# Kernel tuning notes

Measured on AMD Instinct MI355X. Metric: run time of the kernel, lower is better.

Reference implementation:

```python
import jax, jax.numpy as jnp
import numpy as np

B, S, L, CIN = 8, 32, 128, 1024
C1, C2 = 512, 256            # conv1_channel, conv2_channel
D1, D2 = 512, 128            # deconv1_channel, deconv2_channel
CD, SIM = 300, 128           # concept_dim, similarity_dim
L4 = L // 4


def _conv1d(x, w, b, pad):
    # x: [N, Cin, L], w: [Cout, Cin, k] (PyTorch layout)
    y = jax.lax.conv_general_dilated(x, w, (1,), [(pad, pad)],
                                     dimension_numbers=('NCH', 'OIH', 'NCH'))
    return y + b[None, :, None]


def _maxpool2(x):
    return jax.lax.reduce_window(x, -jnp.inf, jax.lax.max, (1, 1, 2), (1, 1, 2), 'VALID')


def _deconv1d(x, w, b):
    # PyTorch ConvTranspose1d(kernel=4, stride=2, padding=1); w: [Cin, Cout, k]
    w2 = jnp.flip(w, -1).transpose(1, 0, 2)  # -> OIH
    y = jax.lax.conv_general_dilated(x, w2, (1,), [(2, 2)], lhs_dilation=(2,),
                                     dimension_numbers=('NCH', 'OIH', 'NCH'))
    return y + b[None, :, None]


def setup_inputs():
    ks = jax.random.split(jax.random.key(0), 32)
    g = lambda i, shape: jax.random.normal(ks[i], shape, jnp.float32) * 0.02
    return {
        'batch': jax.random.normal(ks[0], (B, S, L, CIN), jnp.float32),
        'concept1': jax.random.normal(ks[1], (B, CD), jnp.float32),
        'concept2': jax.random.normal(ks[2], (B, CD), jnp.float32),
        'seg_len': jax.random.randint(ks[3], (B, S), 1, L + 1),
        'conv1_w': g(4, (C1, CIN, 5)), 'conv1_b': g(5, (C1,)),
        'conv2_w': g(6, (C2, C1, 5)), 'conv2_b': g(7, (C2,)),
        'sa_wq': g(8, (C2, C2)), 'sa_bq': g(9, (C2,)),
        'sa_wk': g(10, (C2, C2)), 'sa_bk': g(11, (C2,)),
        'sa_v': g(12, (C2,)), 'sa_vb': g(13, ()),
        'ca_wq': g(14, (CD, C2)), 'ca_bq': g(15, (C2,)),
        'ca_wk': g(16, (C2, C2)), 'ca_bk': g(17, (C2,)),
        'ca_v': g(18, (C2,)), 'ca_vb': g(19, ()),
        'dc1_w': g(20, (4 * C2, D1, 4)), 'dc1_b': g(21, (D1,)),
        'dc2_w': g(22, (D1, D2, 4)), 'dc2_b': g(23, (D2,)),
        'sim1_w': g(24, (D2, SIM)),
        'sim2_w': g(25, (CD, SIM)),
        'mlp_w': g(26, (SIM,)), 'mlp_b': g(27, ()),
    }


def reference(batch, concept1, concept2, seg_len,
              conv1_w, conv1_b, conv2_w, conv2_b,
              sa_wq, sa_bq, sa_wk, sa_bk, sa_v, sa_vb,
              ca_wq, ca_bq, ca_wk, ca_bk, ca_v, ca_vb,
              dc1_w, dc1_b, dc2_w, dc2_b,
              sim1_w, sim2_w, mlp_w, mlp_b):
    N = B * S
    # conv stack: [N, CIN, L] -> [N, C2, L/4]
    x = batch.reshape(N, L, CIN).transpose(0, 2, 1)
    t = _maxpool2(_conv1d(x, conv1_w, conv1_b, 2))
    t = _maxpool2(_conv1d(t, conv2_w, conv2_b, 2))
    tmp2 = t.transpose(0, 2, 1)                       # [N, L4, C2]

    # vectorized length mask: mask[i,j,k] = k < ceil(seg_len/4)  <=>  seg_len > 4k
    mask = (seg_len[:, :, None] > 4 * jnp.arange(L4)).reshape(N, 1, L4)

    # self additive attention over pooled positions
    qp = tmp2 @ sa_wq + sa_bq                          # [N, L4, H]
    kp = tmp2 @ sa_wk + sa_bk                          # [N, L4, H]
    s = jnp.einsum('nqkh,h->nqk', jnp.tanh(qp[:, :, None, :] + kp[:, None, :, :]), sa_v) + sa_vb
    s = jnp.where(mask, s, -1e9)
    a = jax.nn.softmax(s, axis=-1)                     # [N, L4, L4]
    self_res = jnp.einsum('nqk,nkc->nqc', a, tmp2)     # [N, L4, C2]

    # concept attention (query identical across positions -> compute once)
    ckp = tmp2 @ ca_wk + ca_bk                         # [N, L4, H]

    def concept_attn(c):
        cq = jnp.repeat(c @ ca_wq + ca_bq, S, axis=0)  # [N, H]
        sc = jnp.einsum('nkh,h->nk', jnp.tanh(cq[:, None, :] + ckp), ca_v) + ca_vb
        sc = jnp.where(mask[:, 0, :], sc, -1e9)
        ac = jax.nn.softmax(sc, axis=-1)               # [N, L4]
        r = jnp.einsum('nk,nkc->nc', ac, tmp2)         # [N, C2]
        return jnp.broadcast_to(r[:, None, :], (N, L4, C2))

    c1_res = concept_attn(concept1)
    c2_res = concept_attn(concept2)

    ar = jnp.concatenate([tmp2, self_res, c1_res, c2_res], axis=-1)  # [N, L4, 4*C2]
    r = _deconv1d(ar.transpose(0, 2, 1), dc1_w, dc1_b)               # [N, D1, L/2]
    r = _deconv1d(r, dc2_w, dc2_b).transpose(0, 2, 1)                # [N, L, D2]
    r = r.reshape(B, S * L, D2)

    sim1 = r @ sim1_w                                                # [B, S*L, SIM]

    def score(c):
        cs = (c @ sim2_w)[:, None, :] * sim1
        return jax.nn.sigmoid(cs @ mlp_w + mlp_b).reshape(B, S, L)

    return score(concept1), score(concept2)
```

## Files before the change

kernel.cpp:

```cpp
#include <hip/hip_runtime.h>
#include <cstdint>

typedef __bf16 bf16;
typedef __bf16 bf16x8 __attribute__((ext_vector_type(8)));
typedef float f32x4 __attribute__((ext_vector_type(4)));

__device__ __forceinline__ void gload_lds16(const void* g, void* l) {
  __builtin_amdgcn_global_load_lds(
      (const __attribute__((address_space(1))) unsigned int*)g,
      (__attribute__((address_space(3))) unsigned int*)l, 16, 0, 0);
}

__device__ __forceinline__ float tanh_fast(float x) {
  float ax = fabsf(x);
  float e = __expf(ax + ax);
  float t = 1.0f - 2.0f / (e + 1.0f);
  return x < 0.0f ? -t : t;
}

template<bool POOL>
__global__ __launch_bounds__(256) void gemm_tap(
    const bf16* __restrict__ A, const bf16* __restrict__ Bt,
    const float* __restrict__ bias, bf16* __restrict__ Out,
    const bf16* __restrict__ zp,
    int snA, int logP, int logCI, int shift0, int ntaps, int cbCount,
    int cbCI, int pairs, int Ktot, int COt, int snO)
{
  __shared__ __align__(16) bf16 Ab[2][4096];
  __shared__ __align__(16) bf16 Bb[2][4096];
  const int tid  = threadIdx.x;
  const int wave = tid >> 6, lane = tid & 63;
  const int wr = wave >> 1, wc = wave & 1;
  const int m0  = blockIdx.x << 7;
  const int co0 = blockIdx.y << 7;
  const int P     = 1 << logP;
  const int Pmask = P - 1;
  const int CI    = 1 << logCI;
  f32x4 acc[4][4] = {};

  const int rowL = tid >> 2;
  const int kg   = tid & 3;
  const int fOff = ((kg ^ ((rowL + (rowL >> 2)) & 3)) << 3);
  bf16* dA0r0 = &Ab[0][wave * 512];
  bf16* dA0r1 = &Ab[0][2048 + wave * 512];
  bf16* dA1r0 = &Ab[1][wave * 512];
  bf16* dA1r1 = &Ab[1][2048 + wave * 512];
  bf16* dB0r0 = &Bb[0][wave * 512];
  bf16* dB0r1 = &Bb[0][2048 + wave * 512];
  bf16* dB1r0 = &Bb[1][wave * 512];
  bf16* dB1r1 = &Bb[1][2048 + wave * 512];

  const int mA0 = m0 + rowL,      nA0 = mA0 >> logP, pA0v = mA0 & Pmask;
  const int mA1 = m0 + rowL + 64, nA1 = mA1 >> logP, pA1v = mA1 & Pmask;
  const bf16* baseA0 = A + nA0 * snA + fOff;
  const bf16* baseA1 = A + nA1 * snA + fOff;
  const bf16* baseB0 = Bt + (co0 + rowL) * Ktot + fOff;
  const bf16* baseB1 = Bt + (co0 + rowL + 64) * Ktot + fOff;
  const bf16* zsrc = zp + fOff;

  const int frow  = lane & 15;
  const int rdOff = (((lane >> 4) ^ ((frow + (frow >> 2)) & 3)) << 3);

  for (int cb = 0; cb < cbCount; ++cb) {
    for (int tap = 0; tap < ntaps; ++tap) {
      const int sh = tap + shift0;
      const int rA0 = pA0v + sh, rA1 = pA1v + sh;
      const bool v0 = (unsigned)rA0 < (unsigned)P;
      const bool v1 = (unsigned)rA1 < (unsigned)P;
      const bf16* pa0 = v0 ? (baseA0 + rA0 * CI + cb * cbCI) : zsrc;
      const bf16* pa1 = v1 ? (baseA1 + rA1 * CI + cb * cbCI) : zsrc;
      const bf16* pb0 = baseB0 + (cb * ntaps + tap) * cbCI;
      const bf16* pb1 = baseB1 + (cb * ntaps + tap) * cbCI;

      for (int kc = 0; kc < pairs; ++kc) {
        gload_lds16(pa0,      dA0r0);
        gload_lds16(pa0 + 32, dA1r0);
        gload_lds16(pa1,      dA0r1);
        gload_lds16(pa1 + 32, dA1r1);
        gload_lds16(pb0,      dB0r0);
        gload_lds16(pb0 + 32, dB1r0);
        gload_lds16(pb1,      dB0r1);
        gload_lds16(pb1 + 32, dB1r1);
        if (v0) pa0 += 64;
        if (v1) pa1 += 64;
        pb0 += 64; pb1 += 64;
        __syncthreads();
#pragma unroll
        for (int h = 0; h < 2; ++h) {
          bf16x8 af[4], bg[4];
#pragma unroll
          for (int i = 0; i < 4; ++i) {
            af[i] = *(const bf16x8*)&Ab[h][((wr << 6) + (i << 4) + frow) * 32 + rdOff];
            bg[i] = *(const bf16x8*)&Bb[h][((wc << 6) + (i << 4) + frow) * 32 + rdOff];
          }
#pragma unroll
          for (int i = 0; i < 4; ++i)
#pragma unroll
            for (int j = 0; j < 4; ++j)
              acc[i][j] = __builtin_amdgcn_mfma_f32_16x16x32_bf16(af[i], bg[j], acc[i][j], 0, 0, 0);
        }
        __syncthreads();
      }
    }
  }

  const int colL = lane & 15;
  const int rq   = (lane >> 4) << 2;
#pragma unroll
  for (int i = 0; i < 4; ++i) {
    int m = m0 + (wr << 6) + (i << 4) + rq;
    int n = m >> logP, p = m & Pmask;
#pragma unroll
    for (int j = 0; j < 4; ++j) {
      int gco = co0 + (wc << 6) + (j << 4) + colL;
      float bv = bias[gco];
      if (POOL) {
        float v0 = fmaxf(acc[i][j][0], acc[i][j][1]) + bv;
        float v1 = fmaxf(acc[i][j][2], acc[i][j][3]) + bv;
        bf16* o = Out + n * snO + (p >> 1) * COt + gco;
        o[0]   = (bf16)v0;
        o[COt] = (bf16)v1;
      } else {
#pragma unroll
        for (int r = 0; r < 4; ++r)
          Out[n * snO + (p + r) * COt + gco] = (bf16)(acc[i][j][r] + bv);
      }
    }
  }
}

__global__ void kcvt(const float* __restrict__ src, bf16* __restrict__ dst) {
  int idx = (blockIdx.x * 256 + threadIdx.x) * 8;
  float4 a = *(const float4*)&src[idx];
  float4 b = *(const float4*)&src[idx + 4];
  bf16x8 v;
  v[0] = (bf16)a.x; v[1] = (bf16)a.y; v[2] = (bf16)a.z; v[3] = (bf16)a.w;
  v[4] = (bf16)b.x; v[5] = (bf16)b.y; v[6] = (bf16)b.z; v[7] = (bf16)b.w;
  *(bf16x8*)&dst[idx] = v;
}

__global__ __launch_bounds__(256) void prep_all(
    const float* __restrict__ conv1_w, const float* __restrict__ conv2_w,
    const float* __restrict__ sa_wq, const float* __restrict__ sa_wk,
    const float* __restrict__ ca_wk, const float* __restrict__ dc1_w,
    const float* __restrict__ dc2_w, const float* __restrict__ sim1_w,
    const float* __restrict__ c1b, const float* __restrict__ c2b,
    const float* __restrict__ sabq, const float* __restrict__ sabk,
    const float* __restrict__ cabk, const float* __restrict__ d1b,
    const float* __restrict__ d2b,
    const float* __restrict__ c1, const float* __restrict__ c2,
    const float* __restrict__ ca_wq, const float* __restrict__ ca_bq,
    const float* __restrict__ sim2_w, const float* __restrict__ mlp_w,
    bf16* __restrict__ Bt1, bf16* __restrict__ Bt2, bf16* __restrict__ Bqkc,
    bf16* __restrict__ Btd1, bf16* __restrict__ Btd2, bf16* __restrict__ Bts1,
    float* __restrict__ bias, float* __restrict__ cq, float* __restrict__ uu)
{
  const int blk = blockIdx.x;
  if (blk < 27468) {
    int idx = blk * 256 + threadIdx.x;
    if (idx < 3072) {
      if (idx < 2944) {
        float v;
        if (idx < 512)       v = c1b[idx];
        else if (idx < 768)  v = c2b[idx - 512];
        else if (idx < 1024) v = sabq[idx - 768];
        else if (idx < 1280) v = sabk[idx - 1024];
        else if (idx < 1536) v = cabk[idx - 1280];
        else if (idx < 2560) v = d1b[(idx - 1536) & 511];
        else if (idx < 2816) v = d2b[(idx - 2560) & 127];
        else                 v = 0.0f;
        bias[idx] = v;
      }
    } else if (idx < 2624512) {
      int i = idx - 3072;
      int co = i / 5120, r = i - co * 5120;
      int cb = r / 1280, r2 = r - cb * 1280;
      int tap = r2 >> 8, cl = r2 & 255;
      Bt1[i] = (bf16)conv1_w[co * 5120 + (cb * 256 + cl) * 5 + tap];
    } else if (idx < 3279872) {
      int i = idx - 2624512;
      int co = i / 2560, r = i - co * 2560;
      int cb = r / 1280, r2 = r - cb * 1280;
      int tap = r2 >> 8, cl = r2 & 255;
      Bt2[i] = (bf16)conv2_w[co * 2560 + (cb * 256 + cl) * 5 + tap];
    } else if (idx < 3476480) {
      int i = idx - 3279872;
      int co = i >> 8, ci = i & 255;
      float v;
      if (co < 256)      v = sa_wq[ci * 256 + co];
      else if (co < 512) v = sa_wk[ci * 256 + (co - 256)];
      else               v = ca_wk[ci * 256 + (co - 512)];
      Bqkc[i] = (bf16)v;
    } else if (idx < 6622208) {
      int i = idx - 3476480;
      int co = i / 3072, r = i - co * 3072;
      int cb = r / 768, r2 = r - cb * 768;
      int tap = r2 >> 8, cl = r2 & 255;
      int ci = cb * 256 + cl;
      int par = co >> 9, c = co & 511;
      int ki = -1;
      if (par == 0) { if (tap == 1) ki = 1; else if (tap == 0) ki = 3; }
      else          { if (tap == 2) ki = 0; else if (tap == 1) ki = 2; }
      Btd1[i] = (ki >= 0) ? (bf16)dc1_w[ci * 2048 + c * 4 + ki] : (bf16)0.0f;
    } else if (idx < 7015424) {
      int i = idx - 6622208;
      int co = i / 1536, r = i - co * 1536;
      int cb = r / 768, r2 = r - cb * 768;
      int tap = r2 >> 8, cl = r2 & 255;
      int ci = cb * 256 + cl;
      int par = co >> 7, c = co & 127;
      int ki = -1;
      if (par == 0) { if (tap == 1) ki = 1; else if (tap == 0) ki = 3; }
      else          { if (tap == 2) ki = 0; else if (tap == 1) ki = 2; }
      Btd2[i] = (ki >= 0) ? (bf16)dc2_w[ci * 512 + c * 4 + ki] : (bf16)0.0f;
    } else {
      int i = idx - 7015424;
      int co = i >> 7, ci = i & 127;
      Bts1[i] = (bf16)sim1_w[ci * 128 + co];
    }
  } else {
    int sub = blk - 27468;
    if (sub < 16) {
      int o = sub * 256 + threadIdx.x;
      int c = o >> 11, b = (o >> 8) & 7, h = o & 255;
      const float* cc = (c ? c2 : c1) + b * 300;
      float acc = ca_bq[h];
      for (int j = 0; j < 300; ++j)
        acc += cc[j] * ca_wq[j * 256 + h];
      cq[o] = acc;
    } else {
      int o = (sub - 16) * 256 + threadIdx.x;
      int c = o >> 10, b = (o >> 7) & 7, m = o & 127;
      const float* cc = (c ? c2 : c1) + b * 300;
      float acc = 0.0f;
      for (int j = 0; j < 300; ++j)
        acc += cc[j] * sim2_w[j * 128 + m];
      uu[o] = acc * mlp_w[m];
    }
  }
}

__global__ __launch_bounds__(256) void kattn(
    const bf16* __restrict__ tmp2, const bf16* __restrict__ qkc,
    const float* __restrict__ sa_v, const float* __restrict__ sa_vb,
    const float* __restrict__ ca_v, const float* __restrict__ ca_vb,
    const float* __restrict__ cq, const int* __restrict__ seg,
    bf16* __restrict__ ar)
{
  const int n = blockIdx.x, tid = threadIdx.x;
  __shared__ __align__(16) bf16 t2[32 * 264];
  __shared__ __align__(16) bf16 bufA[32 * 264];
  __shared__ __align__(16) bf16 bufB[32 * 264];
  __shared__ float sv_s[256], cv_s[256];
  __shared__ float sbc[66];
  __shared__ float sbs[32 * 33];
  const int sl = seg[n];

#pragma unroll
  for (int rr = 0; rr < 4; ++rr) {
    int q = tid + (rr << 8);
    int k = q >> 5, c8 = (q & 31) << 3;
    *(uint4*)&t2[k * 264 + c8]   = *(const uint4*)&tmp2[n * 8192 + k * 256 + c8];
    *(uint4*)&bufA[k * 264 + c8] = *(const uint4*)&qkc[n * 24576 + k * 768 + 512 + c8];
  }
  sv_s[tid] = sa_v[tid];
  cv_s[tid] = ca_v[tid];
  __syncthreads();

  if (tid < 64) {
    int c = tid >> 5, k = tid & 31;
    const float* cqr = cq + (c * 8 + (n >> 5)) * 256;
    float acc = 0.0f;
    for (int h = 0; h < 256; ++h)
      acc += tanh_fast(cqr[h] + (float)bufA[k * 264 + h]) * cv_s[h];
    float sc = acc + ca_vb[0];
    sbc[c * 33 + k] = (sl > (k << 2)) ? sc : -1e9f;
  }
  __syncthreads();

#pragma unroll
  for (int rr = 0; rr < 4; ++rr) {
    int q = tid + (rr << 8);
    int k = q >> 5, c8 = (q & 31) << 3;
    *(uint4*)&bufB[k * 264 + c8] = *(const uint4*)&qkc[n * 24576 + k * 768 + c8];
    *(uint4*)&bufA[k * 264 + c8] = *(const uint4*)&qkc[n * 24576 + k * 768 + 256 + c8];
  }
  if (tid < 2) {
    float* row = &sbc[tid * 33];
    float mx = -1e30f;
    for (int k = 0; k < 32; ++k) mx = fmaxf(mx, row[k]);
    float sum = 0.0f;
    for (int k = 0; k < 32; ++k) { float e = __expf(row[k] - mx); row[k] = e; sum += e; }
    float inv = 1.0f / sum;
    for (int k = 0; k < 32; ++k) row[k] *= inv;
  }
  __syncthreads();

  {
    int col = tid;
    float rr0 = 0.0f, rr1 = 0.0f;
    for (int k = 0; k < 32; ++k) {
      float tv = (float)t2[k * 264 + col];
      rr0 += sbc[k] * tv;
      rr1 += sbc[33 + k] * tv;
    }
    bf16 b0 = (bf16)rr0, b1 = (bf16)rr1;
    bf16* arn = ar + n * 32768;
    for (int q = 0; q < 32; ++q) {
      arn[q * 1024 + col]       = t2[q * 264 + col];
      arn[q * 1024 + 512 + col] = b0;
      arn[q * 1024 + 768 + col] = b1;
    }
  }
  {
    float svb = sa_vb[0];
#pragma unroll
    for (int rr = 0; rr < 4; ++rr) {
      int id = tid + (rr << 8);
      int q = id >> 5, k = id & 31;
      float acc = 0.0f;
      for (int h = 0; h < 256; ++h)
        acc += tanh_fast((float)bufB[q * 264 + h] + (float)bufA[k * 264 + h]) * sv_s[h];
      float sc = acc + svb;
      sbs[q * 33 + k] = (sl > (k << 2)) ? sc : -1e9f;
    }
  }
  __syncthreads();

  if (tid < 32) {
    float* row = &sbs[tid * 33];
    float mx = -1e30f;
    for (int k = 0; k < 32; ++k) mx = fmaxf(mx, row[k]);
    float sum = 0.0f;
    for (int k = 0; k < 32; ++k) { float e = __expf(row[k] - mx); row[k] = e; sum += e; }
    float inv = 1.0f / sum;
    for (int k = 0; k < 32; ++k) row[k] *= inv;
  }
  __syncthreads();

  {
    int col = tid;
    bf16* arn = ar + n * 32768;
    for (int q = 0; q < 32; ++q) {
      float acc = 0.0f;
      for (int k = 0; k < 32; ++k)
        acc += sbs[q * 33 + k] * (float)t2[k * 264 + col];
      arn[q * 1024 + 256 + col] = (bf16)acc;
    }
  }
}

__global__ __launch_bounds__(256) void kscore(
    const bf16* __restrict__ sim1, const float* __restrict__ uu,
    const float* __restrict__ mlp_b, float* __restrict__ out)
{
  int row = blockIdx.x * 256 + threadIdx.x;
  int b = row >> 12;
  const float* u0 = uu + b * 128;
  const float* u1 = uu + 1024 + b * 128;
  const bf16* sr = sim1 + row * 128;
  float d0 = 0.0f, d1 = 0.0f;
  for (int mm = 0; mm < 128; mm += 8) {
    bf16x8 v = *(const bf16x8*)&sr[mm];
#pragma unroll
    for (int t = 0; t < 8; ++t) {
      float sv = (float)v[t];
      d0 += sv * u0[mm + t];
      d1 += sv * u1[mm + t];
    }
  }
  float bb = mlp_b[0];
  out[row]         = 1.0f / (1.0f + __expf(-(d0 + bb)));
  out[32768 + row] = 1.0f / (1.0f + __expf(-(d1 + bb)));
}

extern "C" void kernel_launch(void* const* d_in, const int* in_sizes, int n_in,
                              void* d_out, int out_size, void* d_ws, size_t ws_size,
                              hipStream_t stream) {
  const float* batch    = (const float*)d_in[0];
  const float* concept1 = (const float*)d_in[1];
  const float* concept2 = (const float*)d_in[2];
  const int*   seg      = (const int*)d_in[3];
  const float* conv1_w  = (const float*)d_in[4];
  const float* conv1_b  = (const float*)d_in[5];
  const float* conv2_w  = (const float*)d_in[6];
  const float* conv2_b  = (const float*)d_in[7];
  const float* sa_wq    = (const float*)d_in[8];
  const float* sa_bq    = (const float*)d_in[9];
  const float* sa_wk    = (const float*)d_in[10];
  const float* sa_bk    = (const float*)d_in[11];
  const float* sa_v     = (const float*)d_in[12];
  const float* sa_vb    = (const float*)d_in[13];
  const float* ca_wq    = (const float*)d_in[14];
  const float* ca_bq    = (const float*)d_in[15];
  const float* ca_wk    = (const float*)d_in[16];
  const float* ca_bk    = (const float*)d_in[17];
  const float* ca_v     = (const float*)d_in[18];
  const float* ca_vb    = (const float*)d_in[19];
  const float* dc1_w    = (const float*)d_in[20];
  const float* dc1_b    = (const float*)d_in[21];
  const float* dc2_w    = (const float*)d_in[22];
  const float* dc2_b    = (const float*)d_in[23];
  const float* sim1_w   = (const float*)d_in[24];
  const float* sim2_w   = (const float*)d_in[25];
  const float* mlp_w    = (const float*)d_in[26];
  const float* mlp_b    = (const float*)d_in[27];

  char* ws = (char*)d_ws;
  bf16* bb16  = (bf16*)(ws + 0);
  bf16* qkcb  = (bf16*)(ws + 0);
  bf16* arb   = (bf16*)(ws + 12582912);
  bf16* d1    = (bf16*)(ws + 29360128);
  bf16* rbuf  = (bf16*)(ws + 46137344);
  bf16* sim1b = (bf16*)(ws + 54525952);
  bf16* t1    = (bf16*)(ws + 67108864);
  bf16* tmp2b = (bf16*)(ws + 83886080);
  bf16* Bt1   = (bf16*)(ws + 88080384);
  bf16* Bt2   = (bf16*)(ws + 93323264);
  bf16* Bqkc  = (bf16*)(ws + 94633984);
  bf16* Btd1  = (bf16*)(ws + 95027200);
  bf16* Btd2  = (bf16*)(ws + 101318656);
  bf16* Bts1  = (bf16*)(ws + 102105088);
  float* biasall = (float*)(ws + 102137856);
  float* cqb  = (float*)(ws + 102149632);
  float* uub  = (float*)(ws + 102166016);
  const bf16* zp = (const bf16*)(biasall + 2816);
  float* outp = (float*)d_out;

  prep_all<<<27492, 256, 0, stream>>>(
      conv1_w, conv2_w, sa_wq, sa_wk, ca_wk, dc1_w, dc2_w, sim1_w,
      conv1_b, conv2_b, sa_bq, sa_bk, ca_bk, dc1_b, dc2_b,
      concept1, concept2, ca_wq, ca_bq, sim2_w, mlp_w,
      Bt1, Bt2, Bqkc, Btd1, Btd2, Bts1, biasall, cqb, uub);

  kcvt<<<16384, 256, 0, stream>>>(batch, bb16);

  gemm_tap<true><<<dim3(256, 4), 256, 0, stream>>>(
      bb16, Bt1, biasall + 0, t1, zp, 131072, 7, 10, -2, 5, 4, 256, 4, 5120, 512, 32768);

  gemm_tap<true><<<dim3(128, 2), 256, 0, stream>>>(
      t1, Bt2, biasall + 512, tmp2b, zp, 32768, 6, 9, -2, 5, 2, 256, 4, 2560, 256, 8192);

  gemm_tap<false><<<dim3(64, 6), 256, 0, stream>>>(
      tmp2b, Bqkc, biasall + 768, qkcb, zp, 8192, 5, 8, 0, 1, 1, 256, 4, 256, 768, 24576);

  kattn<<<256, 256, 0, stream>>>(tmp2b, qkcb, sa_v, sa_vb, ca_v, ca_vb, cqb, seg, arb);

  gemm_tap<false><<<dim3(64, 8), 256, 0, stream>>>(
      arb, Btd1, biasall + 1536, d1, zp, 32768, 5, 10, -1, 3, 4, 256, 4, 3072, 1024, 32768);

  gemm_tap<false><<<dim3(128, 2), 256, 0, stream>>>(
      d1, Btd2, biasall + 2560, rbuf, zp, 32768, 6, 9, -1, 3, 2, 256, 4, 1536, 256, 16384);

  gemm_tap<false><<<dim3(256, 1), 256, 0, stream>>>(
      rbuf, Bts1, biasall + 2816, sim1b, zp, 16384, 7, 7, 0, 1, 1, 128, 2, 128, 128, 16384);

  kscore<<<128, 256, 0, stream>>>(sim1b, uub, mlp_b, outp);
}
```

Baseline: 757.3 us.

## Fuse score into sim1 GEMM, merge batch cast into prep, deepen K-steps

Three changes. The sim1 GEMM epilogue now does the per-row dot with the concept vectors and the sigmoid directly, so the bf16 sim1 buffer is never written and the separate kscore kernel is gone. The fp32-to-bf16 conversion of the input batch moves into extra blocks of the prep kernel, which saves one launch. The GEMM gains a DEPTH parameter that loads 2*DEPTH K-slices per barrier pair for the smaller GEMMs, halving syncthreads at the cost of double LDS use (64 KB), which may lower occupancy.

```diff
diff --git a/kernel.cpp b/kernel.cpp
--- a/kernel.cpp
+++ b/kernel.cpp
@@ -18,16 +18,18 @@
   return x < 0.0f ? -t : t;
 }
 
-template<bool POOL>
+template<int MODE, int DEPTH>
 __global__ __launch_bounds__(256) void gemm_tap(
     const bf16* __restrict__ A, const bf16* __restrict__ Bt,
     const float* __restrict__ bias, bf16* __restrict__ Out,
     const bf16* __restrict__ zp,
     int snA, int logP, int logCI, int shift0, int ntaps, int cbCount,
-    int cbCI, int pairs, int Ktot, int COt, int snO)
+    int cbCI, int pairs, int Ktot, int COt, int snO,
+    const float* __restrict__ uu, const float* __restrict__ mlpb,
+    float* __restrict__ outF)
 {
-  __shared__ __align__(16) bf16 Ab[2][4096];
-  __shared__ __align__(16) bf16 Bb[2][4096];
+  __shared__ __align__(16) bf16 Ab[2 * DEPTH][4096];
+  __shared__ __align__(16) bf16 Bb[2 * DEPTH][4096];
   const int tid  = threadIdx.x;
   const int wave = tid >> 6, lane = tid & 63;
   const int wr = wave >> 1, wc = wave & 1;
@@ -41,14 +43,6 @@
   const int rowL = tid >> 2;
   const int kg   = tid & 3;
   const int fOff = ((kg ^ ((rowL + (rowL >> 2)) & 3)) << 3);
-  bf16* dA0r0 = &Ab[0][wave * 512];
-  bf16* dA0r1 = &Ab[0][2048 + wave * 512];
-  bf16* dA1r0 = &Ab[1][wave * 512];
-  bf16* dA1r1 = &Ab[1][2048 + wave * 512];
-  bf16* dB0r0 = &Bb[0][wave * 512];
-  bf16* dB0r1 = &Bb[0][2048 + wave * 512];
-  bf16* dB1r0 = &Bb[1][wave * 512];
-  bf16* dB1r1 = &Bb[1][2048 + wave * 512];
 
   const int mA0 = m0 + rowL,      nA0 = mA0 >> logP, pA0v = mA0 & Pmask;
   const int mA1 = m0 + rowL + 64, nA1 = mA1 >> logP, pA1v = mA1 & Pmask;
@@ -72,21 +66,20 @@
       const bf16* pb0 = baseB0 + (cb * ntaps + tap) * cbCI;
       const bf16* pb1 = baseB1 + (cb * ntaps + tap) * cbCI;
 
-      for (int kc = 0; kc < pairs; ++kc) {
-        gload_lds16(pa0,      dA0r0);
-        gload_lds16(pa0 + 32, dA1r0);
-        gload_lds16(pa1,      dA0r1);
-        gload_lds16(pa1 + 32, dA1r1);
-        gload_lds16(pb0,      dB0r0);
-        gload_lds16(pb0 + 32, dB1r0);
-        gload_lds16(pb1,      dB0r1);
-        gload_lds16(pb1 + 32, dB1r1);
-        if (v0) pa0 += 64;
-        if (v1) pa1 += 64;
-        pb0 += 64; pb1 += 64;
+      for (int kc = 0; kc < pairs; kc += DEPTH) {
+#pragma unroll
+        for (int h = 0; h < 2 * DEPTH; ++h) {
+          gload_lds16(pa0 + 32 * h, &Ab[h][wave * 512]);
+          gload_lds16(pa1 + 32 * h, &Ab[h][2048 + wave * 512]);
+          gload_lds16(pb0 + 32 * h, &Bb[h][wave * 512]);
+          gload_lds16(pb1 + 32 * h, &Bb[h][2048 + wave * 512]);
+        }
+        if (v0) pa0 += 64 * DEPTH;
+        if (v1) pa1 += 64 * DEPTH;
+        pb0 += 64 * DEPTH; pb1 += 64 * DEPTH;
         __syncthreads();
 #pragma unroll
-        for (int h = 0; h < 2; ++h) {
+        for (int h = 0; h < 2 * DEPTH; ++h) {
           bf16x8 af[4], bg[4];
 #pragma unroll
           for (int i = 0; i < 4; ++i) {
@@ -106,6 +99,44 @@
 
   const int colL = lane & 15;
   const int rq   = (lane >> 4) << 2;
+
+  if (MODE == 2) {
+    float* scr0 = (float*)&Ab[0][0];
+    float* scr1 = (float*)&Bb[0][0];
+    const int n = m0 >> logP;
+    const int b = n >> 5;
+    const float* u0 = uu + b * 128;
+    const float* u1 = uu + 1024 + b * 128;
+#pragma unroll
+    for (int i = 0; i < 4; ++i) {
+#pragma unroll
+      for (int r = 0; r < 4; ++r) {
+        int rowLcl = (wr << 6) + (i << 4) + rq + r;
+        float p0 = 0.0f, p1 = 0.0f;
+#pragma unroll
+        for (int j = 0; j < 4; ++j) {
+          int gco = (wc << 6) + (j << 4) + colL;
+          float v = acc[i][j][r];
+          p0 += v * u0[gco];
+          p1 += v * u1[gco];
+        }
+        scr0[rowLcl * 32 + (wc << 4) + colL] = p0;
+        scr1[rowLcl * 32 + (wc << 4) + colL] = p1;
+      }
+    }
+    __syncthreads();
+    {
+      int rowLcl = tid >> 1, c = tid & 1;
+      const float* s = c ? scr1 : scr0;
+      float sum = 0.0f;
+#pragma unroll
+      for (int k = 0; k < 32; ++k) sum += s[rowLcl * 32 + k];
+      float val = 1.0f / (1.0f + __expf(-(sum + mlpb[0])));
+      outF[(c ? 32768 : 0) + m0 + rowLcl] = val;
+    }
+    return;
+  }
+
 #pragma unroll
   for (int i = 0; i < 4; ++i) {
     int m = m0 + (wr << 6) + (i << 4) + rq;
@@ -114,7 +145,7 @@
     for (int j = 0; j < 4; ++j) {
       int gco = co0 + (wc << 6) + (j << 4) + colL;
       float bv = bias[gco];
-      if (POOL) {
+      if (MODE == 1) {
         float v0 = fmaxf(acc[i][j][0], acc[i][j][1]) + bv;
         float v1 = fmaxf(acc[i][j][2], acc[i][j][3]) + bv;
         bf16* o = Out + n * snO + (p >> 1) * COt + gco;
@@ -127,16 +158,6 @@
       }
     }
   }
-}
-
-__global__ void kcvt(const float* __restrict__ src, bf16* __restrict__ dst) {
-  int idx = (blockIdx.x * 256 + threadIdx.x) * 8;
-  float4 a = *(const float4*)&src[idx];
-  float4 b = *(const float4*)&src[idx + 4];
-  bf16x8 v;
-  v[0] = (bf16)a.x; v[1] = (bf16)a.y; v[2] = (bf16)a.z; v[3] = (bf16)a.w;
-  v[4] = (bf16)b.x; v[5] = (bf16)b.y; v[6] = (bf16)b.z; v[7] = (bf16)b.w;
-  *(bf16x8*)&dst[idx] = v;
 }
 
 __global__ __launch_bounds__(256) void prep_all(
@@ -151,11 +172,22 @@
     const float* __restrict__ c1, const float* __restrict__ c2,
     const float* __restrict__ ca_wq, const float* __restrict__ ca_bq,
     const float* __restrict__ sim2_w, const float* __restrict__ mlp_w,
+    const float* __restrict__ batch, bf16* __restrict__ bb16,
     bf16* __restrict__ Bt1, bf16* __restrict__ Bt2, bf16* __restrict__ Bqkc,
     bf16* __restrict__ Btd1, bf16* __restrict__ Btd2, bf16* __restrict__ Bts1,
     float* __restrict__ bias, float* __restrict__ cq, float* __restrict__ uu)
 {
   const int blk = blockIdx.x;
+  if (blk >= 27492) {
+    int idx = ((blk - 27492) * 256 + threadIdx.x) * 8;
+    float4 a = *(const float4*)&batch[idx];
+    float4 b = *(const float4*)&batch[idx + 4];
+    bf16x8 v;
+    v[0] = (bf16)a.x; v[1] = (bf16)a.y; v[2] = (bf16)a.z; v[3] = (bf16)a.w;
+    v[4] = (bf16)b.x; v[5] = (bf16)b.y; v[6] = (bf16)b.z; v[7] = (bf16)b.w;
+    *(bf16x8*)&bb16[idx] = v;
+    return;
+  }
   if (blk < 27468) {
     int idx = blk * 256 + threadIdx.x;
     if (idx < 3072) {
@@ -350,30 +382,6 @@
   }
 }
 
-__global__ __launch_bounds__(256) void kscore(
-    const bf16* __restrict__ sim1, const float* __restrict__ uu,
-    const float* __restrict__ mlp_b, float* __restrict__ out)
-{
-  int row = blockIdx.x * 256 + threadIdx.x;
-  int b = row >> 12;
-  const float* u0 = uu + b * 128;
-  const float* u1 = uu + 1024 + b * 128;
-  const bf16* sr = sim1 + row * 128;
-  float d0 = 0.0f, d1 = 0.0f;
-  for (int mm = 0; mm < 128; mm += 8) {
-    bf16x8 v = *(const bf16x8*)&sr[mm];
-#pragma unroll
-    for (int t = 0; t < 8; ++t) {
-      float sv = (float)v[t];
-      d0 += sv * u0[mm + t];
-      d1 += sv * u1[mm + t];
-    }
-  }
-  float bb = mlp_b[0];
-  out[row]         = 1.0f / (1.0f + __expf(-(d0 + bb)));
-  out[32768 + row] = 1.0f / (1.0f + __expf(-(d1 + bb)));
-}
-
 extern "C" void kernel_launch(void* const* d_in, const int* in_sizes, int n_in,
                               void* d_out, int out_size, void* d_ws, size_t ws_size,
                               hipStream_t stream) {
@@ -412,7 +420,6 @@
   bf16* arb   = (bf16*)(ws + 12582912);
   bf16* d1    = (bf16*)(ws + 29360128);
   bf16* rbuf  = (bf16*)(ws + 46137344);
-  bf16* sim1b = (bf16*)(ws + 54525952);
   bf16* t1    = (bf16*)(ws + 67108864);
   bf16* tmp2b = (bf16*)(ws + 83886080);
   bf16* Bt1   = (bf16*)(ws + 88080384);
@@ -427,33 +434,36 @@
   const bf16* zp = (const bf16*)(biasall + 2816);
   float* outp = (float*)d_out;
 
-  prep_all<<<27492, 256, 0, stream>>>(
+  prep_all<<<43876, 256, 0, stream>>>(
       conv1_w, conv2_w, sa_wq, sa_wk, ca_wk, dc1_w, dc2_w, sim1_w,
       conv1_b, conv2_b, sa_bq, sa_bk, ca_bk, dc1_b, dc2_b,
       concept1, concept2, ca_wq, ca_bq, sim2_w, mlp_w,
+      batch, bb16,
       Bt1, Bt2, Bqkc, Btd1, Btd2, Bts1, biasall, cqb, uub);
 
-  kcvt<<<16384, 256, 0, stream>>>(batch, bb16);
-
-  gemm_tap<true><<<dim3(256, 4), 256, 0, stream>>>(
-      bb16, Bt1, biasall + 0, t1, zp, 131072, 7, 10, -2, 5, 4, 256, 4, 5120, 512, 32768);
-
-  gemm_tap<true><<<dim3(128, 2), 256, 0, stream>>>(
-      t1, Bt2, biasall + 512, tmp2b, zp, 32768, 6, 9, -2, 5, 2, 256, 4, 2560, 256, 8192);
-
-  gemm_tap<false><<<dim3(64, 6), 256, 0, stream>>>(
-      tmp2b, Bqkc, biasall + 768, qkcb, zp, 8192, 5, 8, 0, 1, 1, 256, 4, 256, 768, 24576);
+  gemm_tap<1, 1><<<dim3(256, 4), 256, 0, stream>>>(
+      bb16, Bt1, biasall + 0, t1, zp, 131072, 7, 10, -2, 5, 4, 256, 4, 5120, 512, 32768,
+      nullptr, nullptr, nullptr);
+
+  gemm_tap<1, 2><<<dim3(128, 2), 256, 0, stream>>>(
+      t1, Bt2, biasall + 512, tmp2b, zp, 32768, 6, 9, -2, 5, 2, 256, 4, 2560, 256, 8192,
+      nullptr, nullptr, nullptr);
+
+  gemm_tap<0, 2><<<dim3(64, 6), 256, 0, stream>>>(
+      tmp2b, Bqkc, biasall + 768, qkcb, zp, 8192, 5, 8, 0, 1, 1, 256, 4, 256, 768, 24576,
+      nullptr, nullptr, nullptr);
 
   kattn<<<256, 256, 0, stream>>>(tmp2b, qkcb, sa_v, sa_vb, ca_v, ca_vb, cqb, seg, arb);
 
-  gemm_tap<false><<<dim3(64, 8), 256, 0, stream>>>(
-      arb, Btd1, biasall + 1536, d1, zp, 32768, 5, 10, -1, 3, 4, 256, 4, 3072, 1024, 32768);
-
-  gemm_tap<false><<<dim3(128, 2), 256, 0, stream>>>(
-      d1, Btd2, biasall + 2560, rbuf, zp, 32768, 6, 9, -1, 3, 2, 256, 4, 1536, 256, 16384);
-
-  gemm_tap<false><<<dim3(256, 1), 256, 0, stream>>>(
-      rbuf, Bts1, biasall + 2816, sim1b, zp, 16384, 7, 7, 0, 1, 1, 128, 2, 128, 128, 16384);
-
-  kscore<<<128, 256, 0, stream>>>(sim1b, uub, mlp_b, outp);
-}
+  gemm_tap<0, 2><<<dim3(64, 8), 256, 0, stream>>>(
+      arb, Btd1, biasall + 1536, d1, zp, 32768, 5, 10, -1, 3, 4, 256, 4, 3072, 1024, 32768,
+      nullptr, nullptr, nullptr);
+
+  gemm_tap<0, 2><<<dim3(128, 2), 256, 0, stream>>>(
+      d1, Btd2, biasall + 2560, rbuf, zp, 32768, 6, 9, -1, 3, 2, 256, 4, 1536, 256, 16384,
+      nullptr, nullptr, nullptr);
+
+  gemm_tap<2, 2><<<dim3(256, 1), 256, 0, stream>>>(
+      rbuf, Bts1, biasall + 2816, nullptr, zp, 16384, 7, 7, 0, 1, 1, 128, 2, 128, 128, 16384,
+      uub, mlp_b, outp);
+}
```

Result: faster. 714.8 us (-5.6%).
